# Optimization experiments

Measured on AMD Instinct MI355X. Metric: run time of the kernel, lower is better.

The kernel has to match this reference:

```python
import jax, jax.numpy as jnp
import numpy as np

P = 2          # feature power
K = 128        # top-k neighbors
ALPHA = 1.0
BETA = 1.0
EPS = 1e-12


def _smooth_rank_l2(v):
    # v: [B, r]. torch: relu(-(v[:,None,:] - v[:,:,None])).sum(-1)
    # element [b,i,j] of diff = v[b,j] - v[b,i]; relu(-diff) = relu(v[b,i]-v[b,j])
    return jnp.sum(jax.nn.relu(v[:, :, None] - v[:, None, :]), axis=-1)  # [B, r]


def setup_inputs() -> dict:
    key = jax.random.key(0)
    k1, k2, k3 = jax.random.split(key, 3)
    B, d, N0 = 256, 2048, 7936
    return {
        "f_s": jax.random.normal(k1, (B, d), dtype=jnp.float32),
        "f_t": jax.random.normal(k2, (B, d), dtype=jnp.float32),
        "gallery": jax.random.normal(k3, (N0, d), dtype=jnp.float32),
    }


def reference(f_s, f_t, gallery):
    # pool='all': x.pow(p).view(B, -1)
    fs = f_s ** P                      # [B, d]
    ft = f_t ** P                      # [B, d]
    # statistics=True, layer 0: teacher_features = concat(existing, f_t)
    gal = jnp.concatenate([gallery, ft], axis=0)   # [N, d]

    d2 = (jnp.sum(ft * ft, axis=-1, keepdims=True)
          + jnp.sum(gal * gal, axis=-1)[None, :]
          - 2.0 * ft @ gal.T)                       # [B, N]
    tt_dist = jnp.sqrt(jnp.clip(d2, EPS, None))

    # k smallest distances (torch.sort ascending + slice [:k])
    neg_top, top_k_index = jax.lax.top_k(-tt_dist, K)
    t_value = -neg_top                               # [B, K], ascending

    # per-row re-gather of gallery and student-to-gallery distances
    gal_k = gal[top_k_index]                         # [B, K, d]
    s_d2 = (jnp.sum(fs * fs, axis=-1)[:, None]
            + jnp.sum(gal_k * gal_k, axis=-1)
            - 2.0 * jnp.einsum('bd,bkd->bk', fs, gal_k))
    s_value = jnp.sqrt(jnp.clip(s_d2, EPS, None))    # [B, K]

    main_loss = ALPHA * jnp.mean(jnp.abs(s_value[:, 0] - t_value[:, 0]))

    r = K - 1
    t_rank = _smooth_rank_l2(t_value[:, 1:])         # [B, r]
    s_rank = _smooth_rank_l2(s_value[:, 1:])         # [B, r]
    extra_loss = BETA * jnp.mean(jnp.linalg.norm(t_rank - s_rank, axis=1)) / r

    return main_loss + extra_loss
```

## Files before the change

kernel.cpp:

```cpp
#include <hip/hip_runtime.h>
#include <hip/hip_bf16.h>

#define BDIM 256
#define DDIM 2048
#define NGAL 7936
#define NTOT 8192
#define TOPK 128
#define EPSC 1e-12f

typedef __attribute__((ext_vector_type(8))) short bf16x8;
typedef __attribute__((ext_vector_type(4))) float f32x4;
typedef unsigned long long u64;

__device__ __forceinline__ short bfr(float x) {
  unsigned u = __float_as_uint(x);
  unsigned r = (u + 0x7FFFu + ((u >> 16) & 1u)) >> 16;
  return (short)r;
}

__global__ __launch_bounds__(256) void k_prep(
    const float* __restrict__ f_t, const float* __restrict__ f_s,
    short* __restrict__ Abf, short* __restrict__ Bbf,
    float* __restrict__ normA, float* __restrict__ galnorm) {
  int b = blockIdx.x, t = threadIdx.x;
  const float4* t4 = (const float4*)(f_t + (size_t)b * DDIM);
  const float4* s4 = (const float4*)(f_s + (size_t)b * DDIM);
  float st = 0.f, ss = 0.f;
  for (int i = t; i < DDIM / 4; i += 256) {
    float4 v = t4[i];
    float4 q = make_float4(v.x * v.x, v.y * v.y, v.z * v.z, v.w * v.w);
    short4 qb = make_short4(bfr(q.x), bfr(q.y), bfr(q.z), bfr(q.w));
    *(short4*)&Abf[(size_t)b * DDIM + i * 4] = qb;
    *(short4*)&Bbf[(size_t)(NGAL + b) * DDIM + i * 4] = qb;
    st += q.x * q.x + q.y * q.y + q.z * q.z + q.w * q.w;
    float4 u_ = s4[i];
    float4 r = make_float4(u_.x * u_.x, u_.y * u_.y, u_.z * u_.z, u_.w * u_.w);
    *(short4*)&Abf[(size_t)(BDIM + b) * DDIM + i * 4] =
        make_short4(bfr(r.x), bfr(r.y), bfr(r.z), bfr(r.w));
    ss += r.x * r.x + r.y * r.y + r.z * r.z + r.w * r.w;
  }
  for (int off = 32; off; off >>= 1) {
    st += __shfl_xor(st, off);
    ss += __shfl_xor(ss, off);
  }
  __shared__ float red[8];
  int lane = t & 63, wv = t >> 6;
  if (lane == 0) { red[wv] = st; red[4 + wv] = ss; }
  __syncthreads();
  if (t == 0) {
    float a = red[0] + red[1] + red[2] + red[3];
    float c = red[4] + red[5] + red[6] + red[7];
    normA[b] = a;
    galnorm[NGAL + b] = a;
    normA[BDIM + b] = c;
  }
}

__global__ __launch_bounds__(256) void k_galn(
    const float* __restrict__ gallery, short* __restrict__ Bbf,
    float* __restrict__ galnorm) {
  int row = blockIdx.x * 4 + (threadIdx.x >> 6);
  int lane = threadIdx.x & 63;
  const float4* g4 = (const float4*)(gallery + (size_t)row * DDIM);
  float s = 0.f;
  for (int i = lane; i < DDIM / 4; i += 64) {
    float4 v = g4[i];
    *(short4*)&Bbf[(size_t)row * DDIM + i * 4] =
        make_short4(bfr(v.x), bfr(v.y), bfr(v.z), bfr(v.w));
    s += v.x * v.x + v.y * v.y + v.z * v.z + v.w * v.w;
  }
  for (int off = 32; off; off >>= 1) s += __shfl_xor(s, off);
  if (lane == 0) galnorm[row] = s;
}

__global__ __launch_bounds__(256) void k_gemm(
    const short* __restrict__ Abf, const short* __restrict__ Bbf,
    const float* __restrict__ normA, const float* __restrict__ galnorm,
    float* __restrict__ d2) {
  __shared__ short S[2][12288];
  int t = threadIdx.x;
  int n0 = blockIdx.x * 128, m0 = blockIdx.y * 64;
  int lane = t & 63, wid = t >> 6;
  int wm = wid >> 1, wn = wid & 1;

  const short* gb[6];
  int lof[6];
#pragma unroll
  for (int q = 0; q < 6; ++q) {
    int c = t + q * 256;
    int r, j;
    const short* base;
    if (c < 512) {
      r = c >> 3; j = c & 7;
      base = Abf + (size_t)(m0 + r) * DDIM;
    } else {
      int cb = c - 512;
      r = cb >> 3; j = cb & 7;
      base = Bbf + (size_t)(n0 + r) * DDIM;
    }
    gb[q] = base + ((j * 8) ^ ((r & 7) << 3));
    lof[q] = c * 8;
  }

  int fr = lane & 15, fk = (lane >> 4) * 8;
  int axor = (fr & 7) << 3;
  f32x4 acc[2][4] = {};

#define STAGE(buf, kt)                                                       \
  {                                                                          \
    _Pragma("unroll") for (int q = 0; q < 6; ++q)                            \
        __builtin_amdgcn_global_load_lds(                                    \
            (const __attribute__((address_space(1))) void*)(gb[q] + (kt)),   \
            (__attribute__((address_space(3))) void*)(&S[buf][lof[q]]), 16,  \
            0, 0);                                                           \
  }

  STAGE(0, 0);
  __syncthreads();
  int cur = 0;
  for (int it = 0; it < DDIM / 64; ++it) {
    if (it + 1 < DDIM / 64) STAGE(cur ^ 1, (it + 1) * 64);
#pragma unroll
    for (int ks = 0; ks < 2; ++ks) {
      int ko = (ks * 32 + fk) ^ axor;
      bf16x8 av[2], bv[4];
#pragma unroll
      for (int mi = 0; mi < 2; ++mi)
        av[mi] = *(const bf16x8*)&S[cur][(wm * 32 + mi * 16 + fr) * 64 + ko];
#pragma unroll
      for (int ni = 0; ni < 4; ++ni)
        bv[ni] =
            *(const bf16x8*)&S[cur][4096 + (wn * 64 + ni * 16 + fr) * 64 + ko];
#pragma unroll
      for (int mi = 0; mi < 2; ++mi)
#pragma unroll
        for (int ni = 0; ni < 4; ++ni)
          acc[mi][ni] = __builtin_amdgcn_mfma_f32_16x16x32_bf16(
              av[mi], bv[ni], acc[mi][ni], 0, 0, 0);
    }
    __syncthreads();
    cur ^= 1;
  }
  int rrow = (lane >> 4) * 4;
#pragma unroll
  for (int mi = 0; mi < 2; ++mi) {
#pragma unroll
    for (int r = 0; r < 4; ++r) {
      int m = m0 + wm * 32 + mi * 16 + rrow + r;
      float nm = normA[m];
#pragma unroll
      for (int ni = 0; ni < 4; ++ni) {
        int n = n0 + wn * 64 + ni * 16 + fr;
        float v = nm + galnorm[n] - 2.0f * acc[mi][ni][r];
        v = fmaxf(v, EPSC);
        if (m < BDIM && n == NGAL + m) v = EPSC;
        d2[(size_t)m * NTOT + n] = v;
      }
    }
  }
#undef STAGE
}

__global__ __launch_bounds__(256) void k_topk(
    const float* __restrict__ d2, float* __restrict__ t_value,
    float* __restrict__ s_value, int* __restrict__ topidx) {
  __shared__ unsigned rowu[NTOT];
  __shared__ unsigned hist[2][4096];
  __shared__ unsigned wsum[4];
  __shared__ u64 s_pref;
  __shared__ unsigned s_kneed, s_cnt;
  int b = blockIdx.x, t = threadIdx.x;
  int lane = t & 63, w = t >> 6;
  const uint4* r4 = (const uint4*)(d2 + (size_t)b * NTOT);
  uint4* rv4 = (uint4*)rowu;
  for (int i = t; i < NTOT / 4; i += 256) rv4[i] = r4[i];
  if (t == 0) { s_pref = 0; s_kneed = TOPK; s_cnt = 0; }

  const int shs[4] = {33, 21, 9, 0};
  const int bts[4] = {12, 12, 12, 9};
#pragma unroll 1
  for (int p = 0; p < 4; ++p) {
    int sh = shs[p], bits = bts[p];
    unsigned nb = 1u << bits;
    for (int i = t; i < 8192; i += 256) hist[0][i] = 0;
    __syncthreads();
    u64 pref = s_pref;
    unsigned kn = s_kneed;
    int sh_hi = sh + bits;
#pragma unroll 1
    for (int s = 0; s < NTOT / 256; ++s) {
      int i = t + s * 256;
      u64 key = ((u64)rowu[i] << 13) | (unsigned)i;
      if ((key >> sh_hi) == pref)
        atomicAdd(&hist[w & 1][(unsigned)(key >> sh) & (nb - 1)], 1u);
    }
    __syncthreads();
    unsigned nbper = nb >> 8;
    unsigned base = t * nbper, ls = 0;
    for (unsigned j = 0; j < nbper; ++j)
      ls += hist[0][base + j] + hist[1][base + j];
    unsigned incl = ls;
    for (int off = 1; off < 64; off <<= 1) {
      unsigned x = __shfl_up(incl, off);
      if (lane >= off) incl += x;
    }
    if (lane == 63) wsum[w] = incl;
    __syncthreads();
    unsigned woff = 0;
    for (int ww = 0; ww < w; ++ww) woff += wsum[ww];
    incl += woff;
    unsigned excl = incl - ls;
    if (excl < kn && kn <= incl) {
      unsigned re = excl, binj = 0;
      for (unsigned j = 0; j < nbper; ++j) {
        unsigned h = hist[0][base + j] + hist[1][base + j];
        if (kn <= re + h) { binj = base + j; break; }
        re += h;
      }
      s_pref = (pref << bits) | binj;
      s_kneed = kn - re;
    }
    __syncthreads();
  }
  u64 kstar = s_pref;
  const float* srow = d2 + (size_t)(BDIM + b) * NTOT;
#pragma unroll 1
  for (int s = 0; s < NTOT / 256; ++s) {
    int i = t + s * 256;
    unsigned u = rowu[i];
    u64 key = ((u64)u << 13) | (unsigned)i;
    if (key <= kstar) {
      unsigned pos = atomicAdd(&s_cnt, 1u);
      t_value[b * TOPK + pos] = sqrtf(__uint_as_float(u));
      s_value[b * TOPK + pos] = sqrtf(srow[i]);
      topidx[b * TOPK + pos] = i;
    }
  }
}

__global__ __launch_bounds__(128) void k_loss(
    const float* __restrict__ t_value, const float* __restrict__ s_value,
    const int* __restrict__ topidx, float* __restrict__ out) {
  int b = blockIdx.x, t = threadIdx.x;
  float tv = t_value[b * TOPK + t], sv = s_value[b * TOPK + t];
  int idx = topidx[b * TOPK + t];
  u64 key = ((u64)__float_as_uint(tv) << 13) | (unsigned)idx;
  u64 m_ = key;
  for (int off = 1; off < 64; off <<= 1) {
    u64 o = __shfl_xor(m_, off);
    if (o < m_) m_ = o;
  }
  __shared__ u64 wmin[2];
  __shared__ float tvs[TOPK], svs[TOPK], red[2], tm_s, sm_s;
  int lane = t & 63, w = t >> 6;
  if (lane == 0) wmin[w] = m_;
  tvs[t] = tv;
  svs[t] = sv;
  __syncthreads();
  u64 kmin = wmin[0] < wmin[1] ? wmin[0] : wmin[1];
  bool ismin = (key == kmin);
  if (ismin) { tm_s = tv; sm_s = sv; }
  __syncthreads();
  float tmv = tm_s, smv = sm_s;
  float tr = 0.f, sr = 0.f;
  for (int j = 0; j < TOPK; ++j) {
    tr += fmaxf(tv - tvs[j], 0.f);
    sr += fmaxf(sv - svs[j], 0.f);
  }
  tr -= fmaxf(tv - tmv, 0.f);
  sr -= fmaxf(sv - smv, 0.f);
  float d = tr - sr;
  float val = ismin ? 0.f : d * d;
  for (int off = 1; off < 64; off <<= 1) val += __shfl_xor(val, off);
  if (lane == 0) red[w] = val;
  __syncthreads();
  if (t == 0) {
    float sum = red[0] + red[1];
    float contrib = (1.f / 256.f) * fabsf(smv - tmv) +
                    (1.f / (127.f * 256.f)) * sqrtf(sum);
    atomicAdd(out, contrib);
  }
}

extern "C" void kernel_launch(void* const* d_in, const int* in_sizes, int n_in,
                              void* d_out, int out_size, void* d_ws,
                              size_t ws_size, hipStream_t stream) {
  const float* f_s = (const float*)d_in[0];
  const float* f_t = (const float*)d_in[1];
  const float* gallery = (const float*)d_in[2];
  float* out = (float*)d_out;

  float* d2 = (float*)d_ws;
  short* Abf = (short*)(d2 + (size_t)512 * NTOT);
  short* Bbf = Abf + (size_t)512 * DDIM;
  float* normA = (float*)(Bbf + (size_t)NTOT * DDIM);
  float* galnorm = normA + 512;
  float* t_value = galnorm + NTOT;
  float* s_value = t_value + BDIM * TOPK;
  int* topidx = (int*)(s_value + BDIM * TOPK);

  hipMemsetAsync(d_out, 0, sizeof(float), stream);

  k_prep<<<BDIM, 256, 0, stream>>>(f_t, f_s, Abf, Bbf, normA, galnorm);
  k_galn<<<NGAL / 4, 256, 0, stream>>>(gallery, Bbf, galnorm);
  k_gemm<<<dim3(NTOT / 128, 512 / 64), 256, 0, stream>>>(Abf, Bbf, normA,
                                                         galnorm, d2);
  k_topk<<<BDIM, 256, 0, stream>>>(d2, t_value, s_value, topidx);
  k_loss<<<BDIM, 128, 0, stream>>>(t_value, s_value, topidx, out);
}
```

Measured before the change: 174.9 us.

## Split top-k into per-chunk partial selection plus bitonic merge, fuse prep kernels

The per-row radix select over 8192 entries is split into four 2048-entry chunks processed by separate blocks, giving 1024 blocks instead of 256. Each chunk keeps its 128 local smallest as packed keys, and a merge kernel bitonic-sorts the 512 candidates, then computes the loss from the sorted top 128. The gallery and feature prep kernels are merged into one launch. This gives more parallelism and smaller LDS per block, at the cost of an extra candidate buffer and a 512-element bitonic sort with many barriers.

```diff
diff --git a/kernel.cpp b/kernel.cpp
--- a/kernel.cpp
+++ b/kernel.cpp
@@ -18,11 +18,28 @@
   return (short)r;
 }
 
-__global__ __launch_bounds__(256) void k_prep(
+__global__ __launch_bounds__(256) void k_prep_gal(
     const float* __restrict__ f_t, const float* __restrict__ f_s,
-    short* __restrict__ Abf, short* __restrict__ Bbf,
-    float* __restrict__ normA, float* __restrict__ galnorm) {
-  int b = blockIdx.x, t = threadIdx.x;
+    const float* __restrict__ gallery, short* __restrict__ Abf,
+    short* __restrict__ Bbf, float* __restrict__ normA,
+    float* __restrict__ galnorm) {
+  int bx = blockIdx.x, t = threadIdx.x;
+  int lane = t & 63, wv = t >> 6;
+  if (bx < NGAL / 4) {
+    int row = bx * 4 + wv;
+    const float4* g4 = (const float4*)(gallery + (size_t)row * DDIM);
+    float s = 0.f;
+    for (int i = lane; i < DDIM / 4; i += 64) {
+      float4 v = g4[i];
+      *(short4*)&Bbf[(size_t)row * DDIM + i * 4] =
+          make_short4(bfr(v.x), bfr(v.y), bfr(v.z), bfr(v.w));
+      s += v.x * v.x + v.y * v.y + v.z * v.z + v.w * v.w;
+    }
+    for (int off = 32; off; off >>= 1) s += __shfl_xor(s, off);
+    if (lane == 0) galnorm[row] = s;
+    return;
+  }
+  int b = bx - NGAL / 4;
   const float4* t4 = (const float4*)(f_t + (size_t)b * DDIM);
   const float4* s4 = (const float4*)(f_s + (size_t)b * DDIM);
   float st = 0.f, ss = 0.f;
@@ -44,7 +61,6 @@
     ss += __shfl_xor(ss, off);
   }
   __shared__ float red[8];
-  int lane = t & 63, wv = t >> 6;
   if (lane == 0) { red[wv] = st; red[4 + wv] = ss; }
   __syncthreads();
   if (t == 0) {
@@ -54,23 +70,6 @@
     galnorm[NGAL + b] = a;
     normA[BDIM + b] = c;
   }
-}
-
-__global__ __launch_bounds__(256) void k_galn(
-    const float* __restrict__ gallery, short* __restrict__ Bbf,
-    float* __restrict__ galnorm) {
-  int row = blockIdx.x * 4 + (threadIdx.x >> 6);
-  int lane = threadIdx.x & 63;
-  const float4* g4 = (const float4*)(gallery + (size_t)row * DDIM);
-  float s = 0.f;
-  for (int i = lane; i < DDIM / 4; i += 64) {
-    float4 v = g4[i];
-    *(short4*)&Bbf[(size_t)row * DDIM + i * 4] =
-        make_short4(bfr(v.x), bfr(v.y), bfr(v.z), bfr(v.w));
-    s += v.x * v.x + v.y * v.y + v.z * v.z + v.w * v.w;
-  }
-  for (int off = 32; off; off >>= 1) s += __shfl_xor(s, off);
-  if (lane == 0) galnorm[row] = s;
 }
 
 __global__ __launch_bounds__(256) void k_gemm(
@@ -161,44 +160,41 @@
 #undef STAGE
 }
 
-__global__ __launch_bounds__(256) void k_topk(
-    const float* __restrict__ d2, float* __restrict__ t_value,
-    float* __restrict__ s_value, int* __restrict__ topidx) {
-  __shared__ unsigned rowu[NTOT];
-  __shared__ unsigned hist[2][4096];
+__global__ __launch_bounds__(256) void k_part(
+    const float* __restrict__ d2, u64* __restrict__ cand) {
+  __shared__ unsigned rowu[2048];
+  __shared__ unsigned hist[2][2048];
   __shared__ unsigned wsum[4];
   __shared__ u64 s_pref;
   __shared__ unsigned s_kneed, s_cnt;
-  int b = blockIdx.x, t = threadIdx.x;
+  int c = blockIdx.x, b = blockIdx.y, t = threadIdx.x;
   int lane = t & 63, w = t >> 6;
-  const uint4* r4 = (const uint4*)(d2 + (size_t)b * NTOT);
-  uint4* rv4 = (uint4*)rowu;
-  for (int i = t; i < NTOT / 4; i += 256) rv4[i] = r4[i];
+  const uint4* src = (const uint4*)(d2 + (size_t)b * NTOT + c * 2048);
+  ((uint4*)rowu)[t] = src[t];
+  ((uint4*)rowu)[t + 256] = src[t + 256];
   if (t == 0) { s_pref = 0; s_kneed = TOPK; s_cnt = 0; }
-
-  const int shs[4] = {33, 21, 9, 0};
-  const int bts[4] = {12, 12, 12, 9};
 #pragma unroll 1
   for (int p = 0; p < 4; ++p) {
-    int sh = shs[p], bits = bts[p];
-    unsigned nb = 1u << bits;
-    for (int i = t; i < 8192; i += 256) hist[0][i] = 0;
+    int sh = 33 - 11 * p;
+    for (int i = t; i < 4096; i += 256) (&hist[0][0])[i] = 0;
     __syncthreads();
     u64 pref = s_pref;
     unsigned kn = s_kneed;
-    int sh_hi = sh + bits;
-#pragma unroll 1
-    for (int s = 0; s < NTOT / 256; ++s) {
+#pragma unroll
+    for (int s = 0; s < 8; ++s) {
       int i = t + s * 256;
-      u64 key = ((u64)rowu[i] << 13) | (unsigned)i;
-      if ((key >> sh_hi) == pref)
-        atomicAdd(&hist[w & 1][(unsigned)(key >> sh) & (nb - 1)], 1u);
-    }
-    __syncthreads();
-    unsigned nbper = nb >> 8;
-    unsigned base = t * nbper, ls = 0;
-    for (unsigned j = 0; j < nbper; ++j)
-      ls += hist[0][base + j] + hist[1][base + j];
+      u64 key = ((u64)rowu[i] << 11) | (unsigned)i;
+      if ((key >> (sh + 11)) == pref) {
+        unsigned bin = (unsigned)(key >> sh) & 2047u;
+        unsigned slot = ((bin & 7u) << 8) | (bin >> 3);
+        atomicAdd(&hist[w & 1][slot], 1u);
+      }
+    }
+    __syncthreads();
+    unsigned ls = 0;
+#pragma unroll
+    for (int q = 0; q < 8; ++q)
+      ls += hist[0][q * 256 + t] + hist[1][q * 256 + t];
     unsigned incl = ls;
     for (int off = 1; off < 64; off <<= 1) {
       unsigned x = __shfl_up(incl, off);
@@ -212,71 +208,76 @@
     unsigned excl = incl - ls;
     if (excl < kn && kn <= incl) {
       unsigned re = excl, binj = 0;
-      for (unsigned j = 0; j < nbper; ++j) {
-        unsigned h = hist[0][base + j] + hist[1][base + j];
-        if (kn <= re + h) { binj = base + j; break; }
+      for (int q = 0; q < 8; ++q) {
+        unsigned h = hist[0][q * 256 + t] + hist[1][q * 256 + t];
+        if (kn <= re + h) { binj = ((unsigned)t << 3) | (unsigned)q; break; }
         re += h;
       }
-      s_pref = (pref << bits) | binj;
+      s_pref = (pref << 11) | binj;
       s_kneed = kn - re;
     }
     __syncthreads();
   }
   u64 kstar = s_pref;
-  const float* srow = d2 + (size_t)(BDIM + b) * NTOT;
-#pragma unroll 1
-  for (int s = 0; s < NTOT / 256; ++s) {
+  u64* dst = cand + ((size_t)b * 4 + c) * TOPK;
+#pragma unroll
+  for (int s = 0; s < 8; ++s) {
     int i = t + s * 256;
     unsigned u = rowu[i];
-    u64 key = ((u64)u << 13) | (unsigned)i;
+    u64 key = ((u64)u << 11) | (unsigned)i;
     if (key <= kstar) {
       unsigned pos = atomicAdd(&s_cnt, 1u);
-      t_value[b * TOPK + pos] = sqrtf(__uint_as_float(u));
-      s_value[b * TOPK + pos] = sqrtf(srow[i]);
-      topidx[b * TOPK + pos] = i;
-    }
-  }
-}
-
-__global__ __launch_bounds__(128) void k_loss(
-    const float* __restrict__ t_value, const float* __restrict__ s_value,
-    const int* __restrict__ topidx, float* __restrict__ out) {
+      dst[pos] = ((u64)u << 13) | (unsigned)(c * 2048 + i);
+    }
+  }
+}
+
+__global__ __launch_bounds__(256) void k_mloss(
+    const u64* __restrict__ cand, const float* __restrict__ d2,
+    float* __restrict__ out) {
+  __shared__ u64 sk[512];
+  __shared__ float tvs[TOPK], svs[TOPK], red[4];
   int b = blockIdx.x, t = threadIdx.x;
-  float tv = t_value[b * TOPK + t], sv = s_value[b * TOPK + t];
-  int idx = topidx[b * TOPK + t];
-  u64 key = ((u64)__float_as_uint(tv) << 13) | (unsigned)idx;
-  u64 m_ = key;
-  for (int off = 1; off < 64; off <<= 1) {
-    u64 o = __shfl_xor(m_, off);
-    if (o < m_) m_ = o;
-  }
-  __shared__ u64 wmin[2];
-  __shared__ float tvs[TOPK], svs[TOPK], red[2], tm_s, sm_s;
+  sk[t] = cand[(size_t)b * 512 + t];
+  sk[t + 256] = cand[(size_t)b * 512 + 256 + t];
+  __syncthreads();
+  for (int len = 2; len <= 512; len <<= 1) {
+    for (int inc = len >> 1; inc; inc >>= 1) {
+      int low = t & (inc - 1);
+      int i0 = ((t - low) << 1) | low, i1 = i0 + inc;
+      u64 a = sk[i0], c2 = sk[i1];
+      bool asc = (i0 & len) == 0;
+      if ((a > c2) == asc) { sk[i0] = c2; sk[i1] = a; }
+      __syncthreads();
+    }
+  }
+  float tv = 0.f, sv = 0.f;
+  const float* srow = d2 + (size_t)(BDIM + b) * NTOT;
+  if (t < TOPK) {
+    u64 key = sk[t];
+    tv = sqrtf(__uint_as_float((unsigned)(key >> 13)));
+    sv = sqrtf(srow[(unsigned)(key & 8191u)]);
+    tvs[t] = tv;
+    svs[t] = sv;
+  }
+  __syncthreads();
+  float val = 0.f;
+  if (t >= 1 && t < TOPK) {
+    float tr = 0.f, sr = 0.f;
+    for (int j = 1; j < TOPK; ++j) {
+      tr += fmaxf(tv - tvs[j], 0.f);
+      sr += fmaxf(sv - svs[j], 0.f);
+    }
+    float d = tr - sr;
+    val = d * d;
+  }
   int lane = t & 63, w = t >> 6;
-  if (lane == 0) wmin[w] = m_;
-  tvs[t] = tv;
-  svs[t] = sv;
-  __syncthreads();
-  u64 kmin = wmin[0] < wmin[1] ? wmin[0] : wmin[1];
-  bool ismin = (key == kmin);
-  if (ismin) { tm_s = tv; sm_s = sv; }
-  __syncthreads();
-  float tmv = tm_s, smv = sm_s;
-  float tr = 0.f, sr = 0.f;
-  for (int j = 0; j < TOPK; ++j) {
-    tr += fmaxf(tv - tvs[j], 0.f);
-    sr += fmaxf(sv - svs[j], 0.f);
-  }
-  tr -= fmaxf(tv - tmv, 0.f);
-  sr -= fmaxf(sv - smv, 0.f);
-  float d = tr - sr;
-  float val = ismin ? 0.f : d * d;
   for (int off = 1; off < 64; off <<= 1) val += __shfl_xor(val, off);
   if (lane == 0) red[w] = val;
   __syncthreads();
   if (t == 0) {
-    float sum = red[0] + red[1];
-    float contrib = (1.f / 256.f) * fabsf(smv - tmv) +
+    float sum = red[0] + red[1] + red[2] + red[3];
+    float contrib = (1.f / 256.f) * fabsf(svs[0] - tvs[0]) +
                     (1.f / (127.f * 256.f)) * sqrtf(sum);
     atomicAdd(out, contrib);
   }
@@ -295,16 +296,14 @@
   short* Bbf = Abf + (size_t)512 * DDIM;
   float* normA = (float*)(Bbf + (size_t)NTOT * DDIM);
   float* galnorm = normA + 512;
-  float* t_value = galnorm + NTOT;
-  float* s_value = t_value + BDIM * TOPK;
-  int* topidx = (int*)(s_value + BDIM * TOPK);
+  u64* cand = (u64*)(galnorm + NTOT);
 
   hipMemsetAsync(d_out, 0, sizeof(float), stream);
 
-  k_prep<<<BDIM, 256, 0, stream>>>(f_t, f_s, Abf, Bbf, normA, galnorm);
-  k_galn<<<NGAL / 4, 256, 0, stream>>>(gallery, Bbf, galnorm);
+  k_prep_gal<<<NGAL / 4 + BDIM, 256, 0, stream>>>(f_t, f_s, gallery, Abf, Bbf,
+                                                  normA, galnorm);
   k_gemm<<<dim3(NTOT / 128, 512 / 64), 256, 0, stream>>>(Abf, Bbf, normA,
                                                          galnorm, d2);
-  k_topk<<<BDIM, 256, 0, stream>>>(d2, t_value, s_value, topidx);
-  k_loss<<<BDIM, 128, 0, stream>>>(t_value, s_value, topidx, out);
-}
+  k_part<<<dim3(4, BDIM), 256, 0, stream>>>(d2, cand);
+  k_mloss<<<BDIM, 256, 0, stream>>>(cand, d2, out);
+}
```

Result: faster. 159.3 us (-8.9%).
